# Kernel tuning notes

Hardware: AMD Instinct MI355X
Metric: run time of the kernel (lower is better)

The kernel has to match this reference:

```python
import jax, jax.numpy as jnp
import numpy as np

EPS = 1e-8

def _div(n, d):
    # div_with_small_value: d = d if d > eps else eps
    return n / jnp.where(d > EPS, d, EPS)

def _lstm_dir(x, Wih, Whh, bih, bhh):
    # x: (B, L, I) -> (hs (B, L, H), h_last (B, H))
    B, L, _ = x.shape
    H = Whh.shape[1]
    xg = jnp.einsum('bli,gi->blg', x, Wih) + bih + bhh  # (B, L, 4H)
    def step(carry, g):
        h, c = carry
        g = g + h @ Whh.T
        i, f, gg, o = jnp.split(g, 4, axis=-1)
        c = jax.nn.sigmoid(f) * c + jax.nn.sigmoid(i) * jnp.tanh(gg)
        h = jax.nn.sigmoid(o) * jnp.tanh(c)
        return (h, c), h
    init = (jnp.zeros((B, H), x.dtype), jnp.zeros((B, H), x.dtype))
    (hT, _), hs = jax.lax.scan(step, init, jnp.swapaxes(xg, 0, 1))
    return jnp.swapaxes(hs, 0, 1), hT

def _bilstm(x, pf, pb):
    fw, fwT = _lstm_dir(x, *pf)
    bw_r, bwT = _lstm_dir(x[:, ::-1], *pb)
    return fw, bw_r[:, ::-1], fwT, bwT

def _mp_full(v1, v2, w):
    # v1 (B,L,H); v2 (B,H) or (B,L,H); w (P,H) -> (B,L,P)
    wv1 = v1[:, :, None, :] * w                      # (B,L,P,H)
    if v2.ndim == 2:
        wv2 = v2[:, None, None, :] * w               # (B,1,P,H)
    else:
        wv2 = v2[:, :, None, :] * w                  # (B,L,P,H)
    num = jnp.sum(wv1 * wv2, -1)
    den = jnp.linalg.norm(wv1, axis=-1) * jnp.linalg.norm(wv2, axis=-1)
    return num / jnp.maximum(den, EPS)               # torch cosine_similarity eps

def _mp_pairwise(v1, v2, w):
    # v1 (B,L1,H), v2 (B,L2,H), w (P,H) -> (B,L1,L2,P)
    wv1 = w[None, :, None, :] * v1[:, None]          # (B,P,L1,H)
    wv2 = w[None, :, None, :] * v2[:, None]          # (B,P,L2,H)
    n = jnp.einsum('bpld,bpmd->bplm', wv1, wv2)
    d = jnp.linalg.norm(wv1, axis=-1)[..., :, None] * jnp.linalg.norm(wv2, axis=-1)[..., None, :]
    return jnp.transpose(_div(n, d), (0, 2, 3, 1))

def _attention(v1, v2):
    # cosine similarity matrix (B, L1, L2)
    n = jnp.einsum('bld,bmd->blm', v1, v2)
    d = jnp.linalg.norm(v1, axis=-1)[:, :, None] * jnp.linalg.norm(v2, axis=-1)[:, None, :]
    return _div(n, d)

def _forward(emb, cWih_f, cWhh_f, cbih_f, cbhh_f, cWih_b, cWhh_b, cbih_b, cbhh_b,
             aWih_f, aWhh_f, abih_f, abhh_f, aWih_b, aWhh_b, abih_b, abhh_b,
             mp_w1, mp_w2, mp_w3, mp_w4, mp_w5, mp_w6, mp_w7, mp_w8,
             fc1_W, fc1_b, fc2_W, fc2_b, text_a, text_b):
    p = emb[text_a]
    h = emb[text_b]
    cpf_p = (cWih_f, cWhh_f, cbih_f, cbhh_f)
    cpb_p = (cWih_b, cWhh_b, cbih_b, cbhh_b)
    con_p_fw, con_p_bw, _, _ = _bilstm(p, cpf_p, cpb_p)
    con_h_fw, con_h_bw, _, _ = _bilstm(h, cpf_p, cpb_p)
    # full matching
    mv_p_full_fw = _mp_full(con_p_fw, con_h_fw[:, -1], mp_w1)
    mv_p_full_bw = _mp_full(con_p_bw, con_h_bw[:, 0], mp_w2)
    mv_h_full_fw = _mp_full(con_h_fw, con_p_fw[:, -1], mp_w1)
    mv_h_full_bw = _mp_full(con_h_bw, con_p_bw[:, 0], mp_w2)
    # maxpool matching
    mv_max_fw = _mp_pairwise(con_p_fw, con_h_fw, mp_w3)
    mv_max_bw = _mp_pairwise(con_p_bw, con_h_bw, mp_w4)
    mv_p_max_fw = mv_max_fw.max(2); mv_p_max_bw = mv_max_bw.max(2)
    mv_h_max_fw = mv_max_fw.max(1); mv_h_max_bw = mv_max_bw.max(1)
    # attentive matching
    att_fw = _attention(con_p_fw, con_h_fw)          # (B,L1,L2)
    att_bw = _attention(con_p_bw, con_h_bw)
    att_h_fw = con_h_fw[:, None] * att_fw[..., None]     # (B,L1,L2,H)
    att_h_bw = con_h_bw[:, None] * att_bw[..., None]
    att_p_fw = con_p_fw[:, :, None] * att_fw[..., None]  # (B,L1,L2,H)
    att_p_bw = con_p_bw[:, :, None] * att_bw[..., None]
    att_mean_h_fw = _div(att_h_fw.sum(2), att_fw.sum(2, keepdims=True))
    att_mean_h_bw = _div(att_h_bw.sum(2), att_bw.sum(2, keepdims=True))
    att_mean_p_fw = _div(att_p_fw.sum(1), jnp.swapaxes(att_fw.sum(1, keepdims=True), 1, 2))
    att_mean_p_bw = _div(att_p_bw.sum(1), jnp.swapaxes(att_bw.sum(1, keepdims=True), 1, 2))
    mv_p_att_mean_fw = _mp_full(con_p_fw, att_mean_h_fw, mp_w5)
    mv_p_att_mean_bw = _mp_full(con_p_bw, att_mean_h_bw, mp_w6)
    mv_h_att_mean_fw = _mp_full(con_h_fw, att_mean_p_fw, mp_w5)
    mv_h_att_mean_bw = _mp_full(con_h_bw, att_mean_p_bw, mp_w6)
    att_max_h_fw = att_h_fw.max(2); att_max_h_bw = att_h_bw.max(2)
    att_max_p_fw = att_p_fw.max(1); att_max_p_bw = att_p_bw.max(1)
    mv_p_att_max_fw = _mp_full(con_p_fw, att_max_h_fw, mp_w7)
    mv_p_att_max_bw = _mp_full(con_p_bw, att_max_h_bw, mp_w8)
    mv_h_att_max_fw = _mp_full(con_h_fw, att_max_p_fw, mp_w7)
    mv_h_att_max_bw = _mp_full(con_h_bw, att_max_p_bw, mp_w8)
    mv_p = jnp.concatenate([mv_p_full_fw, mv_p_max_fw, mv_p_att_mean_fw, mv_p_att_max_fw,
                            mv_p_full_bw, mv_p_max_bw, mv_p_att_mean_bw, mv_p_att_max_bw], 2)
    mv_h = jnp.concatenate([mv_h_full_fw, mv_h_max_fw, mv_h_att_mean_fw, mv_h_att_max_fw,
                            mv_h_full_bw, mv_h_max_bw, mv_h_att_mean_bw, mv_h_att_max_bw], 2)
    apf = (aWih_f, aWhh_f, abih_f, abhh_f)
    apb = (aWih_b, aWhh_b, abih_b, abhh_b)
    _, _, p_fwT, p_bwT = _bilstm(mv_p, apf, apb)
    _, _, h_fwT, h_bwT = _bilstm(mv_h, apf, apb)
    x = jnp.concatenate([p_fwT, p_bwT, h_fwT, h_bwT], 1)  # (B, 4H)
    x = jnp.tanh(x @ fc1_W.T + fc1_b)
    return x @ fc2_W.T + fc2_b

def setup_inputs() -> dict:
    key = jax.random.key(0)
    ks = jax.random.split(key, 40)
    B, L, V, E, H, P = 16, 128, 30000, 300, 128, 4
    def n(i, shape, s=0.05):
        return jax.random.normal(ks[i], shape, jnp.float32) * s
    inp = {
        'text_a': jax.random.randint(ks[0], (B, L), 0, V, jnp.int32),
        'text_b': jax.random.randint(ks[1], (B, L), 0, V, jnp.int32),
        'emb': n(2, (V, E), 0.1),
        'cWih_f': n(3, (4*H, E)), 'cWhh_f': n(4, (4*H, H)), 'cbih_f': n(5, (4*H,)), 'cbhh_f': n(6, (4*H,)),
        'cWih_b': n(7, (4*H, E)), 'cWhh_b': n(8, (4*H, H)), 'cbih_b': n(9, (4*H,)), 'cbhh_b': n(10, (4*H,)),
        'aWih_f': n(11, (4*H, 8*P)), 'aWhh_f': n(12, (4*H, H)), 'abih_f': n(13, (4*H,)), 'abhh_f': n(14, (4*H,)),
        'aWih_b': n(15, (4*H, 8*P)), 'aWhh_b': n(16, (4*H, H)), 'abih_b': n(17, (4*H,)), 'abhh_b': n(18, (4*H,)),
        'fc1_W': n(19, (2*H, 4*H)), 'fc1_b': n(20, (2*H,)),
        'fc2_W': n(21, (2, 2*H)), 'fc2_b': n(22, (2,)),
    }
    for i in range(1, 9):
        inp[f'mp_w{i}'] = jax.random.uniform(ks[22 + i], (P, H), jnp.float32)
    return inp

def reference(text_a, text_b, emb, cWih_f, cWhh_f, cbih_f, cbhh_f, cWih_b, cWhh_b, cbih_b, cbhh_b,
              aWih_f, aWhh_f, abih_f, abhh_f, aWih_b, aWhh_b, abih_b, abhh_b,
              fc1_W, fc1_b, fc2_W, fc2_b, mp_w1, mp_w2, mp_w3, mp_w4, mp_w5, mp_w6, mp_w7, mp_w8):
    return _forward(emb, cWih_f, cWhh_f, cbih_f, cbhh_f, cWih_b, cWhh_b, cbih_b, cbhh_b,
                    aWih_f, aWhh_f, abih_f, abhh_f, aWih_b, aWhh_b, abih_b, abhh_b,
                    mp_w1, mp_w2, mp_w3, mp_w4, mp_w5, mp_w6, mp_w7, mp_w8,
                    fc1_W, fc1_b, fc2_W, fc2_b, text_a, text_b)
```

## Files before the change

### kernel.cpp

```cpp
#include <hip/hip_runtime.h>

#define B_ 16
#define L_ 128
#define ML_ 2048
#define E_ 300
#define H_ 128
#define G_ 512
#define EPSV 1e-8f

typedef const float* fp;

__device__ __forceinline__ float sigm(float x) { return 1.f / (1.f + __expf(-x)); }
__device__ __forceinline__ float tanh_f(float x) {
  float e = __expf(-2.f * fabsf(x));
  float r = (1.f - e) / (1.f + e);
  return copysignf(r, x);
}
__device__ __forceinline__ float ddiv(float n, float d) {
  return n / (d > EPSV ? d : EPSV);
}

__global__ __launch_bounds__(256) void k_proj(
    fp __restrict__ emb,
    const int* __restrict__ ta, const int* __restrict__ tb,
    fp Wf, fp Wb, fp bihf, fp bhhf, fp bihb, fp bhhb,
    float* __restrict__ xg)
{
  const int z = blockIdx.z;
  const int* txt = (z >> 1) ? tb : ta;
  fp W = (z & 1) ? Wb : Wf;
  fp bih = (z & 1) ? bihb : bihf;
  fp bhh = (z & 1) ? bhhb : bhhf;
  float* out = xg + (size_t)z * ML_ * G_;
  const int m0 = blockIdx.x * 64, n0 = blockIdx.y * 64;
  __shared__ float As[12][64];
  __shared__ float Bs[12][64];
  __shared__ int rowidx[64];
  const int tid = threadIdx.x;
  if (tid < 64) rowidx[tid] = txt[m0 + tid];
  __syncthreads();
  const int tm = tid >> 4, tn = tid & 15;
  float acc[4][4] = {};
  for (int k0 = 0; k0 < 300; k0 += 12) {
    for (int i = tid; i < 768; i += 256) {
      int m = i / 12, k = i - m * 12;
      As[k][m] = emb[(size_t)rowidx[m] * 300 + k0 + k];
    }
    for (int i = tid; i < 768; i += 256) {
      int n = i / 12, k = i - n * 12;
      Bs[k][n] = W[(size_t)(n0 + n) * 300 + k0 + k];
    }
    __syncthreads();
    #pragma unroll
    for (int k = 0; k < 12; ++k) {
      float4 a = *(const float4*)&As[k][tm * 4];
      float4 bv = *(const float4*)&Bs[k][tn * 4];
      float aa[4] = {a.x, a.y, a.z, a.w};
      #pragma unroll
      for (int i = 0; i < 4; ++i) {
        acc[i][0] = fmaf(aa[i], bv.x, acc[i][0]);
        acc[i][1] = fmaf(aa[i], bv.y, acc[i][1]);
        acc[i][2] = fmaf(aa[i], bv.z, acc[i][2]);
        acc[i][3] = fmaf(aa[i], bv.w, acc[i][3]);
      }
    }
    __syncthreads();
  }
  float biasv[4];
  #pragma unroll
  for (int j = 0; j < 4; ++j)
    biasv[j] = bih[n0 + tn * 4 + j] + bhh[n0 + tn * 4 + j];
  #pragma unroll
  for (int i = 0; i < 4; ++i) {
    float* row = out + (size_t)(m0 + tm * 4 + i) * G_ + n0 + tn * 4;
    #pragma unroll
    for (int j = 0; j < 4; ++j) row[j] = acc[i][j] + biasv[j];
  }
}

__global__ __launch_bounds__(512) void k_lstm(
    fp __restrict__ xg, fp Whhf, fp Whhb, float* __restrict__ out)
{
  const int b = blockIdx.x, z = blockIdx.y, dir = z & 1;
  fp Whh = dir ? Whhb : Whhf;
  fp __restrict__ xgz = xg + ((size_t)z * ML_ + (size_t)b * L_) * G_;
  float* __restrict__ outz = out + ((size_t)z * ML_ + (size_t)b * L_) * H_;
  const int j = threadIdx.x;
  float w[128];
  {
    const float4* wp = (const float4*)(Whh + (size_t)j * H_);
    #pragma unroll
    for (int q = 0; q < 32; ++q) {
      float4 u = wp[q];
      w[4*q+0] = u.x; w[4*q+1] = u.y; w[4*q+2] = u.z; w[4*q+3] = u.w;
    }
  }
  __shared__ float hs[128];
  __shared__ float gb[4][128];
  if (j < 128) hs[j] = 0.f;
  float c = 0.f;
  const int grp = j >> 7, gi = j & 127;
  __syncthreads();
  for (int t = 0; t < L_; ++t) {
    const int pos = dir ? (L_ - 1 - t) : t;
    float xv = xgz[(size_t)pos * G_ + j];
    float a0 = 0.f, a1 = 0.f, a2 = 0.f, a3 = 0.f;
    const float4* h4 = (const float4*)hs;
    #pragma unroll
    for (int q = 0; q < 32; ++q) {
      float4 hv = h4[q];
      a0 = fmaf(w[4*q+0], hv.x, a0);
      a1 = fmaf(w[4*q+1], hv.y, a1);
      a2 = fmaf(w[4*q+2], hv.z, a2);
      a3 = fmaf(w[4*q+3], hv.w, a3);
    }
    float acc = xv + ((a0 + a1) + (a2 + a3));
    float av = (grp == 2) ? tanh_f(acc) : sigm(acc);
    gb[grp][gi] = av;
    __syncthreads();
    if (j < 128) {
      float iv = gb[0][j], fv = gb[1][j], gv = gb[2][j], ov = gb[3][j];
      c = fmaf(fv, c, iv * gv);
      float hn = ov * tanh_f(c);
      hs[j] = hn;
      outz[(size_t)pos * H_ + j] = hn;
    }
    __syncthreads();
  }
}

__global__ __launch_bounds__(256) void k_att(
    fp __restrict__ con, fp w3, fp w4,
    float* __restrict__ att, float* __restrict__ ameanh, float* __restrict__ amaxh,
    float* __restrict__ pcpart, float* __restrict__ mv)
{
  const int b = blockIdx.x, dir = blockIdx.y, lt = blockIdx.z;
  const int l0 = lt * 32;
  fp __restrict__ cp = con + ((size_t)dir * B_ + b) * L_ * H_;
  fp __restrict__ ch = con + ((size_t)(2 + dir) * B_ + b) * L_ * H_;
  fp w = dir ? w4 : w3;
  float* __restrict__ attg = att + ((size_t)dir * B_ + b) * L_ * L_;
  __shared__ float cps[32][132];
  __shared__ float chs[32][132];
  __shared__ float w2s[4][128];
  __shared__ float attb[32][33];
  __shared__ float pcb[4][32][33];
  __shared__ float n0l[32], nql[4][32], n0m[32], nqm[4][32], asum_s[32];
  const int tid = threadIdx.x;
  for (int i = tid; i < 512; i += 256) {
    float wv = w[i];
    w2s[i >> 7][i & 127] = wv * wv;
  }
  for (int i = tid; i < 4096; i += 256)
    cps[i >> 7][i & 127] = cp[(size_t)(l0 + (i >> 7)) * H_ + (i & 127)];
  __syncthreads();
  for (int d = tid; d < 160; d += 256) {
    int l = d / 5, q = d - l * 5;
    const float4* vr = (const float4*)&cps[l][0];
    float s = 0.f;
    if (q == 0) {
      #pragma unroll 8
      for (int h4 = 0; h4 < 32; ++h4) {
        float4 v = vr[h4];
        s += v.x*v.x + v.y*v.y + v.z*v.z + v.w*v.w;
      }
      n0l[l] = sqrtf(s);
    } else {
      const float4* wr = (const float4*)&w2s[q - 1][0];
      #pragma unroll 8
      for (int h4 = 0; h4 < 32; ++h4) {
        float4 v = vr[h4]; float4 ww = wr[h4];
        s += v.x*v.x*ww.x + v.y*v.y*ww.y + v.z*v.z*ww.z + v.w*v.w*ww.w;
      }
      nql[q - 1][l] = sqrtf(s);
    }
  }
  const int tl = tid >> 3, t8 = tid & 7;
  float amean_acc[16], amax_acc[16];
  #pragma unroll
  for (int i = 0; i < 16; ++i) { amean_acc[i] = 0.f; amax_acc[i] = -3.4e38f; }
  float asum_reg = 0.f;
  float pmax_reg = -3.4e38f;
  for (int mc = 0; mc < 4; ++mc) {
    __syncthreads();
    for (int i = tid; i < 4096; i += 256)
      chs[i >> 7][i & 127] = ch[(size_t)(mc * 32 + (i >> 7)) * H_ + (i & 127)];
    __syncthreads();
    for (int d = tid; d < 160; d += 256) {
      int m = d / 5, q = d - m * 5;
      const float4* vr = (const float4*)&chs[m][0];
      float s = 0.f;
      if (q == 0) {
        #pragma unroll 8
        for (int h4 = 0; h4 < 32; ++h4) {
          float4 v = vr[h4];
          s += v.x*v.x + v.y*v.y + v.z*v.z + v.w*v.w;
        }
        n0m[m] = sqrtf(s);
      } else {
        const float4* wr = (const float4*)&w2s[q - 1][0];
        #pragma unroll 8
        for (int h4 = 0; h4 < 32; ++h4) {
          float4 v = vr[h4]; float4 ww = wr[h4];
          s += v.x*v.x*ww.x + v.y*v.y*ww.y + v.z*v.z*ww.z + v.w*v.w*ww.w;
        }
        nqm[q - 1][m] = sqrtf(s);
      }
    }
    __syncthreads();
    float a0[4], ap0[4], ap1[4], ap2[4], ap3[4];
    #pragma unroll
    for (int mm = 0; mm < 4; ++mm) { a0[mm]=0.f; ap0[mm]=0.f; ap1[mm]=0.f; ap2[mm]=0.f; ap3[mm]=0.f; }
    #pragma unroll 4
    for (int h4 = 0; h4 < 32; ++h4) {
      const float4 av = *(const float4*)&cps[tl][h4 * 4];
      const float4 q0 = *(const float4*)&w2s[0][h4 * 4];
      const float4 q1 = *(const float4*)&w2s[1][h4 * 4];
      const float4 q2 = *(const float4*)&w2s[2][h4 * 4];
      const float4 q3 = *(const float4*)&w2s[3][h4 * 4];
      #pragma unroll
      for (int mm = 0; mm < 4; ++mm) {
        const float4 cv = *(const float4*)&chs[t8 * 4 + mm][h4 * 4];
        float px = av.x * cv.x, py = av.y * cv.y, pz = av.z * cv.z, pw = av.w * cv.w;
        a0[mm] += (px + py) + (pz + pw);
        ap0[mm] += px * q0.x + py * q0.y + pz * q0.z + pw * q0.w;
        ap1[mm] += px * q1.x + py * q1.y + pz * q1.z + pw * q1.w;
        ap2[mm] += px * q2.x + py * q2.y + pz * q2.z + pw * q2.w;
        ap3[mm] += px * q3.x + py * q3.y + pz * q3.z + pw * q3.w;
      }
    }
    #pragma unroll
    for (int mm = 0; mm < 4; ++mm) {
      const int m = t8 * 4 + mm;
      float attv = ddiv(a0[mm], n0l[tl] * n0m[m]);
      attb[tl][m] = attv;
      attg[(size_t)(l0 + tl) * L_ + mc * 32 + m] = attv;
      pcb[0][tl][m] = ddiv(ap0[mm], nql[0][tl] * nqm[0][m]);
      pcb[1][tl][m] = ddiv(ap1[mm], nql[1][tl] * nqm[1][m]);
      pcb[2][tl][m] = ddiv(ap2[mm], nql[2][tl] * nqm[2][m]);
      pcb[3][tl][m] = ddiv(ap3[mm], nql[3][tl] * nqm[3][m]);
    }
    __syncthreads();
    for (int mq = 0; mq < 32; ++mq) {
      float avv = attb[tl][mq];
      const float4* cr = (const float4*)&chs[mq][t8 * 16];
      #pragma unroll
      for (int i = 0; i < 4; ++i) {
        float4 cv = cr[i];
        float t0 = avv * cv.x, t1 = avv * cv.y, t2 = avv * cv.z, t3 = avv * cv.w;
        amean_acc[4*i+0] += t0; amax_acc[4*i+0] = fmaxf(amax_acc[4*i+0], t0);
        amean_acc[4*i+1] += t1; amax_acc[4*i+1] = fmaxf(amax_acc[4*i+1], t1);
        amean_acc[4*i+2] += t2; amax_acc[4*i+2] = fmaxf(amax_acc[4*i+2], t2);
        amean_acc[4*i+3] += t3; amax_acc[4*i+3] = fmaxf(amax_acc[4*i+3], t3);
      }
    }
    if (tid < 32) {
      float s = 0.f;
      for (int mq = 0; mq < 32; ++mq) s += attb[tid][mq];
      asum_reg += s;
    }
    if (tid < 128) {
      const int p = tid >> 5, q = tid & 31;
      float mx = pmax_reg;
      for (int mq = 0; mq < 32; ++mq) mx = fmaxf(mx, pcb[p][q][mq]);
      pmax_reg = mx;
      float mx2 = -3.4e38f;
      for (int lq = 0; lq < 32; ++lq) mx2 = fmaxf(mx2, pcb[p][lq][q]);
      pcpart[((((size_t)dir * B_ + b) * 4 + lt) * 4 + p) * L_ + mc * 32 + q] = mx2;
    }
    __syncthreads();
  }
  if (tid < 32) asum_s[tid] = asum_reg;
  __syncthreads();
  {
    float den = asum_s[tl]; den = (den > EPSV) ? den : EPSV;
    const size_t base = (((size_t)dir * B_ + b) * L_ + l0 + tl) * H_ + t8 * 16;
    #pragma unroll
    for (int i = 0; i < 16; ++i) {
      ameanh[base + i] = amean_acc[i] / den;
      amaxh[base + i] = amax_acc[i];
    }
  }
  if (tid < 128) {
    const int p = tid >> 5, lq = tid & 31;
    mv[(size_t)(b * L_ + l0 + lq) * 32 + (dir ? 20 : 4) + p] = pmax_reg;
  }
}

__global__ __launch_bounds__(256) void k_col(
    fp __restrict__ con, fp __restrict__ att,
    fp __restrict__ pcpart,
    float* __restrict__ ameanp, float* __restrict__ amaxp, float* __restrict__ mv)
{
  const int b = blockIdx.x, dir = blockIdx.y, mt = blockIdx.z;
  const int m0 = mt * 32;
  fp __restrict__ cp = con + ((size_t)dir * B_ + b) * L_ * H_;
  fp __restrict__ attg = att + ((size_t)dir * B_ + b) * L_ * L_;
  __shared__ float atts[128][33];
  __shared__ float cpc[32][132];
  __shared__ float asum_s[32];
  const int tid = threadIdx.x;
  for (int i = tid; i < 4096; i += 256)
    atts[i >> 5][i & 31] = attg[(size_t)(i >> 5) * L_ + m0 + (i & 31)];
  __syncthreads();
  if (tid < 32) {
    float s = 0.f;
    for (int l = 0; l < 128; ++l) s += atts[l][tid];
    asum_s[tid] = s;
  }
  const int tm = tid >> 3, t8 = tid & 7;
  float mean_acc[16], max_acc[16];
  #pragma unroll
  for (int i = 0; i < 16; ++i) { mean_acc[i] = 0.f; max_acc[i] = -3.4e38f; }
  for (int lc = 0; lc < 4; ++lc) {
    __syncthreads();
    for (int i = tid; i < 4096; i += 256)
      cpc[i >> 7][i & 127] = cp[(size_t)(lc * 32 + (i >> 7)) * H_ + (i & 127)];
    __syncthreads();
    for (int lq = 0; lq < 32; ++lq) {
      float avv = atts[lc * 32 + lq][tm];
      const float4* cr = (const float4*)&cpc[lq][t8 * 16];
      #pragma unroll
      for (int i = 0; i < 4; ++i) {
        float4 cv = cr[i];
        float t0 = avv * cv.x, t1 = avv * cv.y, t2 = avv * cv.z, t3 = avv * cv.w;
        mean_acc[4*i+0] += t0; max_acc[4*i+0] = fmaxf(max_acc[4*i+0], t0);
        mean_acc[4*i+1] += t1; max_acc[4*i+1] = fmaxf(max_acc[4*i+1], t1);
        mean_acc[4*i+2] += t2; max_acc[4*i+2] = fmaxf(max_acc[4*i+2], t2);
        mean_acc[4*i+3] += t3; max_acc[4*i+3] = fmaxf(max_acc[4*i+3], t3);
      }
    }
  }
  __syncthreads();
  {
    float den = asum_s[tm]; den = (den > EPSV) ? den : EPSV;
    const size_t base = (((size_t)dir * B_ + b) * L_ + m0 + tm) * H_ + t8 * 16;
    #pragma unroll
    for (int i = 0; i < 16; ++i) {
      ameanp[base + i] = mean_acc[i] / den;
      amaxp[base + i] = max_acc[i];
    }
  }
  if (tid < 128) {
    const int p = tid >> 5, mq = tid & 31;
    float mx = -3.4e38f;
    #pragma unroll
    for (int lt = 0; lt < 4; ++lt)
      mx = fmaxf(mx, pcpart[((((size_t)dir * B_ + b) * 4 + lt) * 4 + p) * L_ + m0 + mq]);
    mv[(size_t)(ML_ + b * L_ + m0 + mq) * 32 + (dir ? 20 : 4) + p] = mx;
  }
}

__global__ __launch_bounds__(256) void k_mv(
    fp __restrict__ con,
    fp __restrict__ ameanh, fp __restrict__ amaxh,
    fp __restrict__ ameanp, fp __restrict__ amaxp,
    fp w1, fp w2, fp w5, fp w6, fp w7, fp w8,
    float* __restrict__ mv)
{
  int idx = blockIdx.x * 256 + threadIdx.x;
  const int p = idx & 3; int t1 = idx >> 2;
  const int type = t1 % 3; int t2 = t1 / 3;
  const int dir = t2 & 1; int t3 = t2 >> 1;
  const int l = t3 & 127; int t4 = t3 >> 7;
  const int b = t4 & 15; const int side = t4 >> 4;
  const float* v1 = con + (((size_t)(side ? 2 : 0) + dir) * B_ + b) * L_ * H_ + (size_t)l * H_;
  const float* v2;
  if (type == 0) {
    v2 = con + (((size_t)(side ? 0 : 2) + dir) * B_ + b) * L_ * H_ + (size_t)(dir ? 0 : L_ - 1) * H_;
  } else {
    const float* base = (type == 1) ? (side ? ameanp : ameanh) : (side ? amaxp : amaxh);
    v2 = base + (((size_t)dir * B_ + b) * L_ + l) * H_;
  }
  fp w = (type == 0) ? (dir ? w2 : w1) : (type == 1) ? (dir ? w6 : w5) : (dir ? w8 : w7);
  w += p * H_;
  float num = 0.f, s1 = 0.f, s2 = 0.f;
  for (int h = 0; h < H_; ++h) {
    float wv = w[h];
    float a = v1[h] * wv, bb = v2[h] * wv;
    num = fmaf(a, bb, num);
    s1 = fmaf(a, a, s1);
    s2 = fmaf(bb, bb, s2);
  }
  float den = sqrtf(s1) * sqrtf(s2);
  int slot = (type == 0) ? (dir ? 16 : 0) + p : (type == 1) ? (dir ? 24 : 8) + p : (dir ? 28 : 12) + p;
  mv[((size_t)side * ML_ + b * L_ + l) * 32 + slot] = ddiv(num, den);
}

__global__ __launch_bounds__(256) void k_aggproj(
    fp __restrict__ mv,
    fp Wf, fp Wb, fp bihf, fp bhhf, fp bihb, fp bhhb,
    float* __restrict__ xg)
{
  const int z = blockIdx.y, side = z >> 1, dir = z & 1;
  fp W = dir ? Wb : Wf;
  fp bih = dir ? bihb : bihf;
  fp bhh = dir ? bhhb : bhhf;
  const int r0 = blockIdx.x * 8;
  const float* src = mv + ((size_t)side * ML_ + r0) * 32;
  float* out = xg + ((size_t)z * ML_ + r0) * G_;
  __shared__ float mvs[8][32];
  const int tid = threadIdx.x;
  mvs[tid >> 5][tid & 31] = src[tid];
  __syncthreads();
  float w0[32], w1v[32];
  {
    const float4* wp = (const float4*)(W + (size_t)tid * 32);
    #pragma unroll
    for (int q = 0; q < 8; ++q) {
      float4 u = wp[q];
      w0[4*q+0] = u.x; w0[4*q+1] = u.y; w0[4*q+2] = u.z; w0[4*q+3] = u.w;
    }
    const float4* wp2 = (const float4*)(W + (size_t)(tid + 256) * 32);
    #pragma unroll
    for (int q = 0; q < 8; ++q) {
      float4 u = wp2[q];
      w1v[4*q+0] = u.x; w1v[4*q+1] = u.y; w1v[4*q+2] = u.z; w1v[4*q+3] = u.w;
    }
  }
  float bias0 = bih[tid] + bhh[tid];
  float bias1 = bih[tid + 256] + bhh[tid + 256];
  for (int r = 0; r < 8; ++r) {
    float acc0 = bias0, acc1 = bias1;
    #pragma unroll
    for (int k = 0; k < 32; ++k) {
      float xv = mvs[r][k];
      acc0 = fmaf(w0[k], xv, acc0);
      acc1 = fmaf(w1v[k], xv, acc1);
    }
    out[(size_t)r * G_ + tid] = acc0;
    out[(size_t)r * G_ + tid + 256] = acc1;
  }
}

__global__ __launch_bounds__(256) void k_fc(
    fp __restrict__ aggseq,
    fp fc1W, fp fc1b, fp fc2W, fp fc2b,
    float* __restrict__ out)
{
  const int b = blockIdx.x, tid = threadIdx.x;
  __shared__ float x[512];
  __shared__ float y[256];
  for (int i = tid; i < 512; i += 256) {
    int z = i >> 7, h = i & 127;
    int l = (z & 1) ? 0 : (L_ - 1);
    x[i] = aggseq[(((size_t)z * B_ + b) * L_ + l) * H_ + h];
  }
  __syncthreads();
  {
    float acc = fc1b[tid];
    const float4* wr = (const float4*)(fc1W + (size_t)tid * 512);
    const float4* x4 = (const float4*)x;
    #pragma unroll 8
    for (int k4 = 0; k4 < 128; ++k4) {
      float4 u = wr[k4];
      float4 xv = x4[k4];
      acc = fmaf(u.x, xv.x, acc);
      acc = fmaf(u.y, xv.y, acc);
      acc = fmaf(u.z, xv.z, acc);
      acc = fmaf(u.w, xv.w, acc);
    }
    y[tid] = tanh_f(acc);
  }
  __syncthreads();
  if (tid < 2) {
    float acc = fc2b[tid];
    for (int k = 0; k < 256; ++k) acc = fmaf(fc2W[tid * 256 + k], y[k], acc);
    out[b * 2 + tid] = acc;
  }
}

extern "C" void kernel_launch(void* const* d_in, const int* in_sizes, int n_in,
                              void* d_out, int out_size, void* d_ws, size_t ws_size,
                              hipStream_t stream) {
  (void)in_sizes; (void)n_in; (void)out_size; (void)ws_size;
  const int* ta = (const int*)d_in[0];
  const int* tb = (const int*)d_in[1];
  fp emb   = (fp)d_in[2];
  fp cWihf = (fp)d_in[3];
  fp cWhhf = (fp)d_in[4];
  fp cbihf = (fp)d_in[5];
  fp cbhhf = (fp)d_in[6];
  fp cWihb = (fp)d_in[7];
  fp cWhhb = (fp)d_in[8];
  fp cbihb = (fp)d_in[9];
  fp cbhhb = (fp)d_in[10];
  fp aWihf = (fp)d_in[11];
  fp aWhhf = (fp)d_in[12];
  fp abihf = (fp)d_in[13];
  fp abhhf = (fp)d_in[14];
  fp aWihb = (fp)d_in[15];
  fp aWhhb = (fp)d_in[16];
  fp abihb = (fp)d_in[17];
  fp abhhb = (fp)d_in[18];
  fp fc1W  = (fp)d_in[19];
  fp fc1b  = (fp)d_in[20];
  fp fc2W  = (fp)d_in[21];
  fp fc2b  = (fp)d_in[22];
  fp w1 = (fp)d_in[23];
  fp w2 = (fp)d_in[24];
  fp w3 = (fp)d_in[25];
  fp w4 = (fp)d_in[26];
  fp w5 = (fp)d_in[27];
  fp w6 = (fp)d_in[28];
  fp w7 = (fp)d_in[29];
  fp w8 = (fp)d_in[30];

  float* ws = (float*)d_ws;
  float* xg     = ws;
  float* con    = xg     + (size_t)4 * ML_ * G_;
  float* attw   = con    + (size_t)4 * ML_ * H_;
  float* ameanh = attw   + (size_t)2 * B_ * L_ * L_;
  float* amaxh  = ameanh + (size_t)2 * ML_ * H_;
  float* ameanp = amaxh  + (size_t)2 * ML_ * H_;
  float* amaxp  = ameanp + (size_t)2 * ML_ * H_;
  float* pcpart = amaxp  + (size_t)2 * ML_ * H_;
  float* mvb    = pcpart + (size_t)2 * B_ * 16 * L_;
  float* aggseq = mvb    + (size_t)2 * ML_ * 32;

  k_proj<<<dim3(32, 8, 4), 256, 0, stream>>>(emb, ta, tb, cWihf, cWihb,
                                             cbihf, cbhhf, cbihb, cbhhb, xg);
  k_lstm<<<dim3(16, 4), 512, 0, stream>>>(xg, cWhhf, cWhhb, con);
  k_att<<<dim3(16, 2, 4), 256, 0, stream>>>(con, w3, w4, attw, ameanh, amaxh, pcpart, mvb);
  k_col<<<dim3(16, 2, 4), 256, 0, stream>>>(con, attw, pcpart, ameanp, amaxp, mvb);
  k_mv<<<384, 256, 0, stream>>>(con, ameanh, amaxh, ameanp, amaxp, w1, w2, w5, w6, w7, w8, mvb);
  k_aggproj<<<dim3(256, 4), 256, 0, stream>>>(mvb, aWihf, aWihb, abihf, abhhf, abihb, abhhb, xg);
  k_lstm<<<dim3(16, 4), 512, 0, stream>>>(xg, aWhhf, aWhhb, aggseq);
  k_fc<<<16, 256, 0, stream>>>(aggseq, fc1W, fc1b, fc2W, fc2b, (float*)d_out);
}
```

Measured before the change: 485.6 us.

## Restructure LSTM recurrence: two gates per thread, shuffle exchange, single barrier

The LSTM recurrence kernel now uses 256 threads, each computing two gate rows, so 256 weights live in registers per thread. The four gates for a hidden unit sit in lanes 32 apart and are exchanged with wavefront shuffles, which removes the shared gate buffer. With double-buffered hidden state, each timestep needs one barrier instead of two. The next step's input projection is also prefetched a step ahead. The cost is very high register pressure, with a risk of spilling, and a raw barrier that depends on a manual waitcnt.

```diff
diff --git a/kernel.cpp b/kernel.cpp
--- a/kernel.cpp
+++ b/kernel.cpp
@@ -78,54 +78,77 @@
   }
 }
 
-__global__ __launch_bounds__(512) void k_lstm(
+__global__ __launch_bounds__(256, 1) void k_lstm(
     fp __restrict__ xg, fp Whhf, fp Whhb, float* __restrict__ out)
 {
   const int b = blockIdx.x, z = blockIdx.y, dir = z & 1;
   fp Whh = dir ? Whhb : Whhf;
   fp __restrict__ xgz = xg + ((size_t)z * ML_ + (size_t)b * L_) * G_;
   float* __restrict__ outz = out + ((size_t)z * ML_ + (size_t)b * L_) * H_;
-  const int j = threadIdx.x;
-  float w[128];
+  const int tid = threadIdx.x;
+  const int wv = tid >> 6, lane = tid & 63;
+  const int half = lane >> 5;
+  const int j = wv * 32 + (lane & 31);
+  const int g0 = half ? (128 + j) : j;
+  const int g1 = half ? (384 + j) : (256 + j);
+  float4 wA[32], wB[32];
   {
-    const float4* wp = (const float4*)(Whh + (size_t)j * H_);
-    #pragma unroll
-    for (int q = 0; q < 32; ++q) {
-      float4 u = wp[q];
-      w[4*q+0] = u.x; w[4*q+1] = u.y; w[4*q+2] = u.z; w[4*q+3] = u.w;
-    }
-  }
-  __shared__ float hs[128];
-  __shared__ float gb[4][128];
-  if (j < 128) hs[j] = 0.f;
+    const float4* pA = (const float4*)(Whh + (size_t)g0 * H_);
+    const float4* pB = (const float4*)(Whh + (size_t)g1 * H_);
+    #pragma unroll
+    for (int q = 0; q < 32; ++q) wA[q] = pA[q];
+    #pragma unroll
+    for (int q = 0; q < 32; ++q) wB[q] = pB[q];
+  }
+  __shared__ float hs[2][128];
+  if (tid < 128) hs[0][tid] = 0.f;
   float c = 0.f;
-  const int grp = j >> 7, gi = j & 127;
-  __syncthreads();
+  float xvA = xgz[(size_t)(dir ? (L_ - 1) : 0) * G_ + g0];
+  float xvB = xgz[(size_t)(dir ? (L_ - 1) : 0) * G_ + g1];
+  __syncthreads();
+  int cur = 0;
   for (int t = 0; t < L_; ++t) {
     const int pos = dir ? (L_ - 1 - t) : t;
-    float xv = xgz[(size_t)pos * G_ + j];
-    float a0 = 0.f, a1 = 0.f, a2 = 0.f, a3 = 0.f;
-    const float4* h4 = (const float4*)hs;
+    const int tn = (t + 1 < L_) ? (t + 1) : t;
+    const int posn = dir ? (L_ - 1 - tn) : tn;
+    float xvA_n = xgz[(size_t)posn * G_ + g0];
+    float xvB_n = xgz[(size_t)posn * G_ + g1];
+    float a0=0.f,a1=0.f,a2=0.f,a3=0.f;
+    float b0=0.f,b1=0.f,b2=0.f,b3=0.f;
+    const float4* h4 = (const float4*)hs[cur];
     #pragma unroll
     for (int q = 0; q < 32; ++q) {
       float4 hv = h4[q];
-      a0 = fmaf(w[4*q+0], hv.x, a0);
-      a1 = fmaf(w[4*q+1], hv.y, a1);
-      a2 = fmaf(w[4*q+2], hv.z, a2);
-      a3 = fmaf(w[4*q+3], hv.w, a3);
-    }
-    float acc = xv + ((a0 + a1) + (a2 + a3));
-    float av = (grp == 2) ? tanh_f(acc) : sigm(acc);
-    gb[grp][gi] = av;
-    __syncthreads();
-    if (j < 128) {
-      float iv = gb[0][j], fv = gb[1][j], gv = gb[2][j], ov = gb[3][j];
-      c = fmaf(fv, c, iv * gv);
-      float hn = ov * tanh_f(c);
-      hs[j] = hn;
+      float4 va = wA[q], vb = wB[q];
+      a0 = fmaf(va.x, hv.x, a0);
+      a1 = fmaf(va.y, hv.y, a1);
+      a2 = fmaf(va.z, hv.z, a2);
+      a3 = fmaf(va.w, hv.w, a3);
+      b0 = fmaf(vb.x, hv.x, b0);
+      b1 = fmaf(vb.y, hv.y, b1);
+      b2 = fmaf(vb.z, hv.z, b2);
+      b3 = fmaf(vb.w, hv.w, b3);
+    }
+    float accA = xvA + ((a0 + a1) + (a2 + a3));
+    float accB = xvB + ((b0 + b1) + (b2 + b3));
+    float sA = sigm(accA);
+    float sB = half ? sigm(accB) : tanh_f(accB);
+    float pA = __shfl_xor(sA, 32, 64);
+    float pB = __shfl_xor(sB, 32, 64);
+    float iv = half ? pA : sA;
+    float fv = half ? sA : pA;
+    float gv = half ? pB : sB;
+    float ov = half ? sB : pB;
+    c = fmaf(fv, c, iv * gv);
+    float hn = ov * tanh_f(c);
+    const int nxt = cur ^ 1;
+    if (half == 0) {
+      hs[nxt][j] = hn;
       outz[(size_t)pos * H_ + j] = hn;
     }
-    __syncthreads();
+    asm volatile("s_waitcnt lgkmcnt(0)" ::: "memory");
+    __builtin_amdgcn_s_barrier();
+    cur = nxt; xvA = xvA_n; xvB = xvB_n;
   }
 }
 
@@ -520,11 +543,11 @@
 
   k_proj<<<dim3(32, 8, 4), 256, 0, stream>>>(emb, ta, tb, cWihf, cWihb,
                                              cbihf, cbhhf, cbihb, cbhhb, xg);
-  k_lstm<<<dim3(16, 4), 512, 0, stream>>>(xg, cWhhf, cWhhb, con);
+  k_lstm<<<dim3(16, 4), 256, 0, stream>>>(xg, cWhhf, cWhhb, con);
   k_att<<<dim3(16, 2, 4), 256, 0, stream>>>(con, w3, w4, attw, ameanh, amaxh, pcpart, mvb);
   k_col<<<dim3(16, 2, 4), 256, 0, stream>>>(con, attw, pcpart, ameanp, amaxp, mvb);
   k_mv<<<384, 256, 0, stream>>>(con, ameanh, amaxh, ameanp, amaxp, w1, w2, w5, w6, w7, w8, mvb);
   k_aggproj<<<dim3(256, 4), 256, 0, stream>>>(mvb, aWihf, aWihb, abihf, abhhf, abihb, abhhb, xg);
-  k_lstm<<<dim3(16, 4), 512, 0, stream>>>(xg, aWhhf, aWhhb, aggseq);
+  k_lstm<<<dim3(16, 4), 256, 0, stream>>>(xg, aWhhf, aWhhb, aggseq);
   k_fc<<<16, 256, 0, stream>>>(aggseq, fc1W, fc1b, fc2W, fc2b, (float*)d_out);
 }
```

After: 677.9 us. 1.4x slower.

## Restructure LSTM recurrence with wave-local gate exchange and single barrier per step

Applied to the files above, without the earlier changes.

Reorganizes the LSTM recurrent kernel so each lane computes two gate rows over half of the hidden dimension. Partial sums are combined and the i/f/g/o gates exchanged through cross-lane shuffles instead of shared memory. The hidden state is double-buffered so each timestep needs one barrier instead of two, and the next step's input gates are prefetched. It also uses packed FP32 FMA and launch bounds hinting two blocks per CU, which adds register pressure and relies on inline asm for waitcnt/barrier.

```diff
diff --git a/kernel.cpp b/kernel.cpp
--- a/kernel.cpp
+++ b/kernel.cpp
@@ -9,6 +9,7 @@
 #define EPSV 1e-8f
 
 typedef const float* fp;
+typedef __attribute__((ext_vector_type(2))) float f32x2;
 
 __device__ __forceinline__ float sigm(float x) { return 1.f / (1.f + __expf(-x)); }
 __device__ __forceinline__ float tanh_f(float x) {
@@ -18,6 +19,9 @@
 }
 __device__ __forceinline__ float ddiv(float n, float d) {
   return n / (d > EPSV ? d : EPSV);
+}
+__device__ __forceinline__ void pkfma(f32x2& d, f32x2 a, f32x2 b) {
+  asm("v_pk_fma_f32 %0, %1, %2, %0" : "+v"(d) : "v"(a), "v"(b));
 }
 
 __global__ __launch_bounds__(256) void k_proj(
@@ -78,54 +82,79 @@
   }
 }
 
-__global__ __launch_bounds__(512) void k_lstm(
+__global__ __launch_bounds__(512, 2) void k_lstm(
     fp __restrict__ xg, fp Whhf, fp Whhb, float* __restrict__ out)
 {
   const int b = blockIdx.x, z = blockIdx.y, dir = z & 1;
   fp Whh = dir ? Whhb : Whhf;
   fp __restrict__ xgz = xg + ((size_t)z * ML_ + (size_t)b * L_) * G_;
   float* __restrict__ outz = out + ((size_t)z * ML_ + (size_t)b * L_) * H_;
-  const int j = threadIdx.x;
-  float w[128];
+  const int tid = threadIdx.x;
+  const int wv = tid >> 6, l = tid & 63;
+  const int kh = l & 1, ph = (l >> 1) & 1, jj = l >> 2;
+  const int j = wv * 16 + jj;
+  const int rA = ph * H_ + j;
+  const int rB = rA + 2 * H_;
+  f32x2 wA[32], wB[32];
   {
-    const float4* wp = (const float4*)(Whh + (size_t)j * H_);
-    #pragma unroll
-    for (int q = 0; q < 32; ++q) {
-      float4 u = wp[q];
-      w[4*q+0] = u.x; w[4*q+1] = u.y; w[4*q+2] = u.z; w[4*q+3] = u.w;
-    }
-  }
-  __shared__ float hs[128];
-  __shared__ float gb[4][128];
-  if (j < 128) hs[j] = 0.f;
+    const float4* pA = (const float4*)(Whh + (size_t)rA * H_ + kh * 64);
+    const float4* pB = (const float4*)(Whh + (size_t)rB * H_ + kh * 64);
+    float4* dA = (float4*)wA; float4* dB = (float4*)wB;
+    #pragma unroll
+    for (int q = 0; q < 16; ++q) dA[q] = pA[q];
+    #pragma unroll
+    for (int q = 0; q < 16; ++q) dB[q] = pB[q];
+  }
+  __shared__ float hs[2][128];
+  if (tid < 128) hs[0][tid] = 0.f;
   float c = 0.f;
-  const int grp = j >> 7, gi = j & 127;
-  __syncthreads();
+  const int pos0 = dir ? (L_ - 1) : 0;
+  float xvA = xgz[(size_t)pos0 * G_ + rA];
+  float xvB = xgz[(size_t)pos0 * G_ + rB];
+  __syncthreads();
+  int cur = 0;
   for (int t = 0; t < L_; ++t) {
     const int pos = dir ? (L_ - 1 - t) : t;
-    float xv = xgz[(size_t)pos * G_ + j];
-    float a0 = 0.f, a1 = 0.f, a2 = 0.f, a3 = 0.f;
-    const float4* h4 = (const float4*)hs;
-    #pragma unroll
-    for (int q = 0; q < 32; ++q) {
+    const int tnext = (t + 1 < L_) ? (t + 1) : t;
+    const int posn = dir ? (L_ - 1 - tnext) : tnext;
+    float xvA_n = xgz[(size_t)posn * G_ + rA];
+    float xvB_n = xgz[(size_t)posn * G_ + rB];
+    f32x2 accA0 = {0.f, 0.f}, accA1 = {0.f, 0.f};
+    f32x2 accB0 = {0.f, 0.f}, accB1 = {0.f, 0.f};
+    const float4* h4 = (const float4*)(&hs[cur][kh * 64]);
+    #pragma unroll
+    for (int q = 0; q < 16; ++q) {
       float4 hv = h4[q];
-      a0 = fmaf(w[4*q+0], hv.x, a0);
-      a1 = fmaf(w[4*q+1], hv.y, a1);
-      a2 = fmaf(w[4*q+2], hv.z, a2);
-      a3 = fmaf(w[4*q+3], hv.w, a3);
-    }
-    float acc = xv + ((a0 + a1) + (a2 + a3));
-    float av = (grp == 2) ? tanh_f(acc) : sigm(acc);
-    gb[grp][gi] = av;
-    __syncthreads();
-    if (j < 128) {
-      float iv = gb[0][j], fv = gb[1][j], gv = gb[2][j], ov = gb[3][j];
-      c = fmaf(fv, c, iv * gv);
-      float hn = ov * tanh_f(c);
-      hs[j] = hn;
+      f32x2 hlo; hlo.x = hv.x; hlo.y = hv.y;
+      f32x2 hhi; hhi.x = hv.z; hhi.y = hv.w;
+      pkfma(accA0, wA[2 * q],     hlo);
+      pkfma(accA1, wA[2 * q + 1], hhi);
+      pkfma(accB0, wB[2 * q],     hlo);
+      pkfma(accB1, wB[2 * q + 1], hhi);
+    }
+    float aA = (accA0.x + accA0.y) + (accA1.x + accA1.y);
+    float aB = (accB0.x + accB0.y) + (accB1.x + accB1.y);
+    aA += __shfl_xor(aA, 1, 64);
+    aB += __shfl_xor(aB, 1, 64);
+    aA += xvA; aB += xvB;
+    float actA = sigm(aA);
+    float actB = ph ? sigm(aB) : tanh_f(aB);
+    float exA = __shfl_xor(actA, 2, 64);
+    float exB = __shfl_xor(actB, 2, 64);
+    float iv = ph ? exA : actA;
+    float fv = ph ? actA : exA;
+    float gv = ph ? exB : actB;
+    float ov = ph ? actB : exB;
+    c = fmaf(fv, c, iv * gv);
+    float hn = ov * tanh_f(c);
+    const int nxt = cur ^ 1;
+    if ((l & 3) == 0) {
+      hs[nxt][j] = hn;
       outz[(size_t)pos * H_ + j] = hn;
     }
-    __syncthreads();
+    asm volatile("s_waitcnt lgkmcnt(0)" ::: "memory");
+    __builtin_amdgcn_s_barrier();
+    cur = nxt; xvA = xvA_n; xvB = xvB_n;
   }
 }
 
```

After: 503.5 us. 1.04x slower.

## Batch LSTM recurrence across sequences with split-bf16 MFMA matvec

Applied to the files above, without the earlier changes.

The LSTM kernel now runs one workgroup per direction/text pair and processes all 16 batch sequences together. The recurrent h·Whh product becomes a 16x512x128 matrix multiply done with bf16 MFMA instructions. Precision is kept near fp32 by splitting both weights and hidden state into high and low bf16 parts and issuing three MFMAs per tile. The next step's input gates are prefetched, and hidden state is double-buffered in LDS so each step needs only one barrier. In exchange the grid shrinks from 64 workgroups to 4, so far fewer CUs are used, and each step does three times the MFMA work plus extra bf16 conversions.

```diff
diff --git a/kernel.cpp b/kernel.cpp
--- a/kernel.cpp
+++ b/kernel.cpp
@@ -9,6 +9,8 @@
 #define EPSV 1e-8f
 
 typedef const float* fp;
+typedef __attribute__((ext_vector_type(8))) short bf16x8;
+typedef __attribute__((ext_vector_type(4))) float f32x4v;
 
 __device__ __forceinline__ float sigm(float x) { return 1.f / (1.f + __expf(-x)); }
 __device__ __forceinline__ float tanh_f(float x) {
@@ -18,6 +20,14 @@
 }
 __device__ __forceinline__ float ddiv(float n, float d) {
   return n / (d > EPSV ? d : EPSV);
+}
+__device__ __forceinline__ unsigned short bfr(float x) {
+  union { float f; unsigned u; } a; a.f = x;
+  unsigned r = (a.u + 0x7fffu + ((a.u >> 16) & 1u)) >> 16;
+  return (unsigned short)r;
+}
+__device__ __forceinline__ float bf2f(unsigned short h) {
+  union { unsigned u; float f; } a; a.u = ((unsigned)h) << 16; return a.f;
 }
 
 __global__ __launch_bounds__(256) void k_proj(
@@ -78,54 +88,104 @@
   }
 }
 
-__global__ __launch_bounds__(512) void k_lstm(
-    fp __restrict__ xg, fp Whhf, fp Whhb, float* __restrict__ out)
-{
-  const int b = blockIdx.x, z = blockIdx.y, dir = z & 1;
+__global__ __launch_bounds__(512) __attribute__((amdgpu_waves_per_eu(2, 2)))
+void k_lstm(fp __restrict__ xg, fp Whhf, fp Whhb, float* __restrict__ out)
+{
+  const int z = blockIdx.x, dir = z & 1;
   fp Whh = dir ? Whhb : Whhf;
-  fp __restrict__ xgz = xg + ((size_t)z * ML_ + (size_t)b * L_) * G_;
-  float* __restrict__ outz = out + ((size_t)z * ML_ + (size_t)b * L_) * H_;
-  const int j = threadIdx.x;
-  float w[128];
-  {
-    const float4* wp = (const float4*)(Whh + (size_t)j * H_);
-    #pragma unroll
-    for (int q = 0; q < 32; ++q) {
-      float4 u = wp[q];
-      w[4*q+0] = u.x; w[4*q+1] = u.y; w[4*q+2] = u.z; w[4*q+3] = u.w;
-    }
-  }
-  __shared__ float hs[128];
-  __shared__ float gb[4][128];
-  if (j < 128) hs[j] = 0.f;
-  float c = 0.f;
-  const int grp = j >> 7, gi = j & 127;
-  __syncthreads();
+  fp xz = xg + (size_t)z * ML_ * G_;
+  const int tid = threadIdx.x;
+  const int w = tid >> 6, l = tid & 63, m = l & 15, q = l >> 4;
+  bf16x8 wh[4][4], wl[4][4];
+  #pragma unroll
+  for (int tau = 0; tau < 4; ++tau) {
+    const int grow = 16 * (w + 8 * tau) + m;
+    #pragma unroll
+    for (int kk = 0; kk < 4; ++kk) {
+      const float* wp = Whh + (size_t)grow * H_ + kk * 32 + q * 8;
+      #pragma unroll
+      for (int i = 0; i < 8; ++i) {
+        float x = wp[i];
+        unsigned short hh = bfr(x);
+        wh[tau][kk][i] = (short)hh;
+        wl[tau][kk][i] = (short)bfr(x - bf2f(hh));
+      }
+    }
+  }
+  __shared__ unsigned int h2[2][2048];
+  for (int i = tid; i < 2048; i += 512) h2[0][i] = 0u;
+  float cc[4] = {0.f, 0.f, 0.f, 0.f};
+  const int pos0 = dir ? (L_ - 1) : 0;
+  float xc[4][4];
+  #pragma unroll
+  for (int tau = 0; tau < 4; ++tau) {
+    const int grow = 16 * (w + 8 * tau) + m;
+    #pragma unroll
+    for (int r = 0; r < 4; ++r)
+      xc[tau][r] = xz[((size_t)(4 * q + r) * L_ + pos0) * G_ + grow];
+  }
+  __syncthreads();
+  int cur = 0;
+  const int j = 16 * w + m;
+  const unsigned wbase = ((unsigned)((j >> 5) * 4 + ((j >> 3) & 3)) << 7) | (unsigned)(j & 7);
   for (int t = 0; t < L_; ++t) {
     const int pos = dir ? (L_ - 1 - t) : t;
-    float xv = xgz[(size_t)pos * G_ + j];
-    float a0 = 0.f, a1 = 0.f, a2 = 0.f, a3 = 0.f;
-    const float4* h4 = (const float4*)hs;
-    #pragma unroll
-    for (int q = 0; q < 32; ++q) {
-      float4 hv = h4[q];
-      a0 = fmaf(w[4*q+0], hv.x, a0);
-      a1 = fmaf(w[4*q+1], hv.y, a1);
-      a2 = fmaf(w[4*q+2], hv.z, a2);
-      a3 = fmaf(w[4*q+3], hv.w, a3);
-    }
-    float acc = xv + ((a0 + a1) + (a2 + a3));
-    float av = (grp == 2) ? tanh_f(acc) : sigm(acc);
-    gb[grp][gi] = av;
-    __syncthreads();
-    if (j < 128) {
-      float iv = gb[0][j], fv = gb[1][j], gv = gb[2][j], ov = gb[3][j];
-      c = fmaf(fv, c, iv * gv);
-      float hn = ov * tanh_f(c);
-      hs[j] = hn;
-      outz[(size_t)pos * H_ + j] = hn;
-    }
-    __syncthreads();
+    const int tn = (t + 1 < L_) ? t + 1 : t;
+    const int posn = dir ? (L_ - 1 - tn) : tn;
+    float xn[4][4];
+    #pragma unroll
+    for (int tau = 0; tau < 4; ++tau) {
+      const int grow = 16 * (w + 8 * tau) + m;
+      #pragma unroll
+      for (int r = 0; r < 4; ++r)
+        xn[tau][r] = xz[((size_t)(4 * q + r) * L_ + posn) * G_ + grow];
+    }
+    bf16x8 ah[4], al[4];
+    #pragma unroll
+    for (int kk = 0; kk < 4; ++kk) {
+      const uint4* hp = (const uint4*)&h2[cur][(((unsigned)(kk * 4 + q)) << 7) | ((unsigned)m << 3)];
+      uint4 u0 = hp[0], u1 = hp[1];
+      unsigned uu[8] = {u0.x, u0.y, u0.z, u0.w, u1.x, u1.y, u1.z, u1.w};
+      #pragma unroll
+      for (int i = 0; i < 8; ++i) {
+        ah[kk][i] = (short)(uu[i] >> 16);
+        al[kk][i] = (short)(uu[i] & 0xffffu);
+      }
+    }
+    f32x4v acc[4];
+    #pragma unroll
+    for (int tau = 0; tau < 4; ++tau) {
+      #pragma unroll
+      for (int r = 0; r < 4; ++r) acc[tau][r] = xc[tau][r];
+      #pragma unroll
+      for (int kk = 0; kk < 4; ++kk) {
+        acc[tau] = __builtin_amdgcn_mfma_f32_16x16x32_bf16(ah[kk], wh[tau][kk], acc[tau], 0, 0, 0);
+        acc[tau] = __builtin_amdgcn_mfma_f32_16x16x32_bf16(al[kk], wh[tau][kk], acc[tau], 0, 0, 0);
+        acc[tau] = __builtin_amdgcn_mfma_f32_16x16x32_bf16(ah[kk], wl[tau][kk], acc[tau], 0, 0, 0);
+      }
+    }
+    const int nxt = cur ^ 1;
+    #pragma unroll
+    for (int r = 0; r < 4; ++r) {
+      float iv = sigm(acc[0][r]);
+      float fv = sigm(acc[1][r]);
+      float gv = tanh_f(acc[2][r]);
+      float ov = sigm(acc[3][r]);
+      cc[r] = fmaf(fv, cc[r], iv * gv);
+      float hn = ov * tanh_f(cc[r]);
+      out[(((size_t)z * ML_) + (size_t)(4 * q + r) * L_ + pos) * H_ + j] = hn;
+      unsigned short hh = bfr(hn);
+      unsigned short hl = bfr(hn - bf2f(hh));
+      h2[nxt][wbase + ((unsigned)(4 * q + r) << 3)] = ((unsigned)hh << 16) | (unsigned)hl;
+    }
+    asm volatile("s_waitcnt lgkmcnt(0)" ::: "memory");
+    __builtin_amdgcn_s_barrier();
+    cur = nxt;
+    #pragma unroll
+    for (int tau = 0; tau < 4; ++tau) {
+      #pragma unroll
+      for (int r = 0; r < 4; ++r) xc[tau][r] = xn[tau][r];
+    }
   }
 }
 
@@ -520,11 +580,11 @@
 
   k_proj<<<dim3(32, 8, 4), 256, 0, stream>>>(emb, ta, tb, cWihf, cWihb,
                                              cbihf, cbhhf, cbihb, cbhhb, xg);
-  k_lstm<<<dim3(16, 4), 512, 0, stream>>>(xg, cWhhf, cWhhb, con);
+  k_lstm<<<dim3(4), 512, 0, stream>>>(xg, cWhhf, cWhhb, con);
   k_att<<<dim3(16, 2, 4), 256, 0, stream>>>(con, w3, w4, attw, ameanh, amaxh, pcpart, mvb);
   k_col<<<dim3(16, 2, 4), 256, 0, stream>>>(con, attw, pcpart, ameanp, amaxp, mvb);
   k_mv<<<384, 256, 0, stream>>>(con, ameanh, amaxh, ameanp, amaxp, w1, w2, w5, w6, w7, w8, mvb);
   k_aggproj<<<dim3(256, 4), 256, 0, stream>>>(mvb, aWihf, aWihb, abihf, abhhf, abihb, abhhb, xg);
-  k_lstm<<<dim3(16, 4), 512, 0, stream>>>(xg, aWhhf, aWhhb, aggseq);
+  k_lstm<<<dim3(4), 512, 0, stream>>>(xg, aWhhf, aWhhb, aggseq);
   k_fc<<<16, 256, 0, stream>>>(aggseq, fc1W, fc1b, fc2W, fc2b, (float*)d_out);
 }
```

Measured after the change: 855.6 us. 76.2% more time.
